# Kernel tuning notes

Measured on AMD Instinct MI355X. Metric: run time of the kernel, lower is better.

## Reference

```python
import jax, jax.numpy as jnp
import numpy as np

B, N = 4, 1024
D_MODEL, N_HEADS, D_HEAD, D_COORD = 512, 8, 64, 2


def setup_inputs() -> dict:
    key = jax.random.key(0)
    ks = jax.random.split(key, 8)
    sd = 1.0 / np.sqrt(D_MODEL)
    return {
        "x": jax.random.normal(ks[0], (B, N, D_MODEL), dtype=jnp.float32),
        "positions": jax.random.uniform(ks[1], (N, D_COORD), dtype=jnp.float32) * 32.0,
        "W_Q": jax.random.normal(ks[2], (D_MODEL, N_HEADS * D_HEAD), dtype=jnp.float32) * sd,
        "W_K": jax.random.normal(ks[3], (D_MODEL, N_HEADS * D_HEAD), dtype=jnp.float32) * sd,
        "W_V": jax.random.normal(ks[4], (D_MODEL, N_HEADS * D_HEAD), dtype=jnp.float32) * sd,
        "W_O": jax.random.normal(ks[5], (N_HEADS * D_HEAD, D_MODEL), dtype=jnp.float32) * sd,
        "U": jax.random.normal(ks[6], (N_HEADS, D_HEAD, D_HEAD), dtype=jnp.float32),
        "freqs": jax.random.normal(ks[7], (N_HEADS, D_HEAD // 2, D_COORD), dtype=jnp.float32),
    }


def reference(x, positions, W_Q, W_K, W_V, W_O, U, freqs):
    # x: (B,N,d_model); positions: (N,d_coord); U: (H,dh,dh); freqs: (H,m,d_coord)
    Bn, Nn, _ = x.shape
    H, dh, _ = U.shape
    m = dh // 2
    scale = (dh // 2) ** -0.5

    Q = (x @ W_Q).reshape(Bn, Nn, H, dh)
    K = (x @ W_K).reshape(Bn, Nn, H, dh)
    V = (x @ W_V).reshape(Bn, Nn, H, dh)

    # Active-subspace projector: Pi = qr(U)[0] @ qr(U)[0].T per head
    Uq = jax.vmap(lambda u: jnp.linalg.qr(u)[0])(U)              # (H,dh,dh)
    P = jnp.einsum('hde,hfe->hdf', Uq, Uq)                       # U U^T
    Qp = jnp.einsum('bnhd,hdf->bhnf', Q, P)                      # (B,H,N,dh)
    Kp = jnp.einsum('bnhd,hdf->bhnf', K, P)

    # Relative rotation: R_rel(r_j - r_i) is block-diag 2x2 rotations with
    # angle theta_ijm = freqs_m . (r_j - r_i) = a_jm - a_im (separable), so
    # q^T R(r_j-r_i) k = (R(a_i)q)^T (R(a_j)k)  -- exact RoPE identity.
    ang = jnp.einsum('nc,hmc->hnm', positions, freqs)            # (H,N,m)
    c = jnp.cos(ang)[None]                                       # (1,H,N,m)
    s = jnp.sin(ang)[None]

    def rot(v):  # v: (B,H,N,dh) -> rotated (even, odd) halves (B,H,N,m)
        ve, vo = v[..., ::2], v[..., 1::2]
        return ve * c - vo * s, ve * s + vo * c

    qe, qo = rot(Qp)
    ke, ko = rot(Kp)
    scores = (jnp.einsum('bhim,bhjm->bhij', qe, ke)
              + jnp.einsum('bhim,bhjm->bhij', qo, ko)) * scale   # (B,H,N,N)
    w = jax.nn.softmax(scores, axis=-1)
    out = jnp.einsum('bhij,bjhd->bihd', w, V).reshape(Bn, Nn, H * dh)
    return out @ W_O
```

## Files before the change

kernel.cpp:

```cpp
#include <hip/hip_runtime.h>
#include <math.h>

#define NBATCH 4
#define NSEQ   1024
#define DMODEL 512
#define NH     8
#define DH     64
#define MROWS  (NBATCH*NSEQ)
#define MHALF  (DH/2)

typedef __attribute__((ext_vector_type(8))) short bf16x8;
typedef __attribute__((ext_vector_type(4))) float floatx4;

__device__ __forceinline__ ushort f2bf(float f) {
    union { float f; uint u; } v; v.f = f;
    uint r = v.u + 0x7fffu + ((v.u >> 16) & 1u);
    return (ushort)(r >> 16);
}

__global__ __launch_bounds__(256) void prep_kernel(
    const float* __restrict__ pos, const float* __restrict__ freqs,
    const float* __restrict__ x,
    const float* __restrict__ Wq, const float* __restrict__ Wk,
    const float* __restrict__ Wv, const float* __restrict__ Wo,
    float* __restrict__ cosT, float* __restrict__ sinT,
    ushort* __restrict__ xb, ushort* __restrict__ Wt)
{
    __shared__ float T[64][65];
    const int bid = blockIdx.x;
    const int tid = threadIdx.x;

    if (bid < 1024) {
        int idx = bid * 256 + tid;
        int m = idx & 31;
        int n = (idx >> 5) & 1023;
        int h = idx >> 15;
        float a = pos[n*2+0] * freqs[(h*MHALF+m)*2+0]
                + pos[n*2+1] * freqs[(h*MHALF+m)*2+1];
        cosT[idx] = cosf(a);
        sinT[idx] = sinf(a);
    } else if (bid < 2048) {
        int idx = ((bid - 1024) * 256 + tid) * 8;
        float4 a = *(const float4*)&x[idx];
        float4 b = *(const float4*)&x[idx+4];
        uint4 pk;
        pk.x = (uint)f2bf(a.x) | ((uint)f2bf(a.y) << 16);
        pk.y = (uint)f2bf(a.z) | ((uint)f2bf(a.w) << 16);
        pk.z = (uint)f2bf(b.x) | ((uint)f2bf(b.y) << 16);
        pk.w = (uint)f2bf(b.z) | ((uint)f2bf(b.w) << 16);
        *(uint4*)&xb[idx] = pk;
    } else {
        int b2 = bid - 2048;
        int n0g = (b2 & 31) * 64;
        int k0  = (b2 >> 5) * 64;
        int mat = n0g >> 9;
        const float* W = (mat == 0) ? Wq : ((mat == 1) ? Wk : ((mat == 2) ? Wv : Wo));
        int n0 = n0g & 511;
        int c = tid & 63, r = tid >> 6;
        #pragma unroll
        for (int i = 0; i < 16; i++)
            T[r + i*4][c] = W[(k0 + r + i*4) * DMODEL + n0 + c];
        __syncthreads();
        int nl = tid >> 2;
        int kg = tid & 3;
        #pragma unroll
        for (int g = 0; g < 4; g++) {
            int kl = kg * 16 + g * 4;
            uint2 pk;
            pk.x = (uint)f2bf(T[kl+0][nl]) | ((uint)f2bf(T[kl+1][nl]) << 16);
            pk.y = (uint)f2bf(T[kl+2][nl]) | ((uint)f2bf(T[kl+3][nl]) << 16);
            *(uint2*)&Wt[(size_t)(n0g + nl) * DMODEL + k0 + kl] = pk;
        }
    }
}

__global__ __launch_bounds__(256) void qkv_gemm(
    const ushort* __restrict__ xb, const ushort* __restrict__ Wt,
    const float* __restrict__ cosT, const float* __restrict__ sinT,
    ushort* __restrict__ Qb, ushort* __restrict__ Kb, ushort* __restrict__ Vt)
{
    __shared__ ushort As[64 * 40];
    __shared__ ushort Bs[64 * 40];
    __shared__ float  Cs[64][65];

    const int cb = blockIdx.x;
    const int rb = blockIdx.y;
    const int mat = cb >> 3;
    const int c0 = (cb & 7) * 64;
    const int r0 = rb * 64;
    const int ng0 = mat * 512 + c0;

    const int tid = threadIdx.x;
    const int w = tid >> 6, l = tid & 63;
    const int lr = l & 15, lg = l >> 4;

    const int srow = tid >> 2;
    const int sgrp = tid & 3;

    floatx4 acc[4];
    #pragma unroll
    for (int nt = 0; nt < 4; nt++) acc[nt] = (floatx4){0.f,0.f,0.f,0.f};

    for (int k0 = 0; k0 < DMODEL; k0 += 32) {
        __syncthreads();
        *(uint4*)&As[srow*40 + sgrp*8] =
            *(const uint4*)&xb[(size_t)(r0 + srow) * DMODEL + k0 + sgrp*8];
        *(uint4*)&Bs[srow*40 + sgrp*8] =
            *(const uint4*)&Wt[(size_t)(ng0 + srow) * DMODEL + k0 + sgrp*8];
        __syncthreads();

        bf16x8 af = *(const bf16x8*)&As[(16*w + lr)*40 + lg*8];
        #pragma unroll
        for (int nt = 0; nt < 4; nt++) {
            bf16x8 bf = *(const bf16x8*)&Bs[(nt*16 + lr)*40 + lg*8];
            acc[nt] = __builtin_amdgcn_mfma_f32_16x16x32_bf16(af, bf, acc[nt], 0, 0, 0);
        }
    }

    __syncthreads();
    #pragma unroll
    for (int nt = 0; nt < 4; nt++)
        #pragma unroll
        for (int r = 0; r < 4; r++)
            Cs[16*w + lg*4 + r][nt*16 + lr] = acc[nt][r];
    __syncthreads();

    const int tx = tid & 15, ty = tid >> 4;
    const int dbase = tx * 4;
    const int head = c0 >> 6;

    if (mat == 2) {
        int rowbase = r0 + ty * 4;
        int b = rowbase >> 10, n0 = rowbase & 1023;
        size_t vbase = (size_t)(b * NH + head) * DH;
        #pragma unroll
        for (int j = 0; j < 4; j++) {
            ushort us[4];
            #pragma unroll
            for (int i = 0; i < 4; i++) us[i] = f2bf(Cs[ty*4 + i][tx*4 + j]);
            uint2 pk;
            pk.x = (uint)us[0] | ((uint)us[1] << 16);
            pk.y = (uint)us[2] | ((uint)us[3] << 16);
            *(uint2*)&Vt[(vbase + dbase + j) * NSEQ + n0] = pk;
        }
    } else {
        ushort* dst = (mat == 0) ? Qb : Kb;
        #pragma unroll
        for (int i = 0; i < 4; i++) {
            int row = r0 + ty * 4 + i;
            int b = row >> 10, n = row & 1023;
            float v[4];
            #pragma unroll
            for (int p = 0; p < 2; p++) {
                int de = dbase + 2 * p;
                int m = de >> 1;
                float c = cosT[(head * NSEQ + n) * MHALF + m];
                float s = sinT[(head * NSEQ + n) * MHALF + m];
                float ve = Cs[ty*4 + i][tx*4 + 2*p];
                float vo = Cs[ty*4 + i][tx*4 + 2*p + 1];
                v[2*p]     = ve * c - vo * s;
                v[2*p + 1] = ve * s + vo * c;
            }
            uint2 pk;
            pk.x = (uint)f2bf(v[0]) | ((uint)f2bf(v[1]) << 16);
            pk.y = (uint)f2bf(v[2]) | ((uint)f2bf(v[3]) << 16);
            *(uint2*)&dst[((size_t)(b * NH + head) * NSEQ + n) * DH + dbase] = pk;
        }
    }
}

__global__ __launch_bounds__(256, 4) void attn_kernel(
    const ushort* __restrict__ Qb, const ushort* __restrict__ Kb,
    const ushort* __restrict__ Vt, float* __restrict__ Opart,
    float2* __restrict__ Ml)
{
    __shared__ ushort Ks[64 * 72];
    __shared__ ushort Vs[64 * 72];
    __shared__ ushort Ps[64 * 72];

    const int tid = threadIdx.x;
    const int w = tid >> 6, l = tid & 63;
    const int lr = l & 15, lg = l >> 4;
    const int bh = blockIdx.y, q0 = blockIdx.x * 64;
    const int z = blockIdx.z, jt0 = z * 8;

    const ushort* Qg = Qb + (size_t)bh * NSEQ * DH;
    const ushort* Kg = Kb + (size_t)bh * NSEQ * DH;
    const ushort* Vg = Vt + (size_t)bh * DH * NSEQ;

    bf16x8 qf[2];
    #pragma unroll
    for (int ks = 0; ks < 2; ks++)
        qf[ks] = *(const bf16x8*)(Qg + (size_t)(q0 + 16*w + lr) * DH + ks*32 + lg*8);

    floatx4 ot[4];
    #pragma unroll
    for (int i = 0; i < 4; i++) ot[i] = (floatx4){0.f, 0.f, 0.f, 0.f};
    float m_run = -INFINITY, l_run = 0.f;
    const float scale = 0.17677669529663687f;

    const int sr = tid >> 2;
    const int sc = (tid & 3) * 16;

    const ushort* kp = Kg + (size_t)(jt0*64 + sr) * DH + sc;
    uint4 ka  = *(const uint4*)kp;
    uint4 kb2 = *(const uint4*)(kp + 8);
    const ushort* vp = Vg + (size_t)sr * NSEQ + jt0*64 + sc;
    uint4 va  = *(const uint4*)vp;
    uint4 vb2 = *(const uint4*)(vp + 8);

    for (int jt = jt0; jt < jt0 + 8; jt++) {
        __syncthreads();
        *(uint4*)&Ks[sr*72 + sc]     = ka;
        *(uint4*)&Ks[sr*72 + sc + 8] = kb2;
        *(uint4*)&Vs[sr*72 + sc]     = va;
        *(uint4*)&Vs[sr*72 + sc + 8] = vb2;
        __syncthreads();

        if (jt < jt0 + 7) {
            const ushort* kn = Kg + (size_t)((jt+1)*64 + sr) * DH + sc;
            ka  = *(const uint4*)kn;
            kb2 = *(const uint4*)(kn + 8);
            const ushort* vn = Vg + (size_t)sr * NSEQ + (jt+1)*64 + sc;
            va  = *(const uint4*)vn;
            vb2 = *(const uint4*)(vn + 8);
        }

        floatx4 st[4];
        #pragma unroll
        for (int jm = 0; jm < 4; jm++) {
            floatx4 acc = (floatx4){0.f, 0.f, 0.f, 0.f};
            #pragma unroll
            for (int ks = 0; ks < 2; ks++) {
                bf16x8 af = *(const bf16x8*)&Ks[(jm*16 + lr)*72 + ks*32 + lg*8];
                acc = __builtin_amdgcn_mfma_f32_16x16x32_bf16(af, qf[ks], acc, 0, 0, 0);
            }
            st[jm] = acc;
        }

        float mx = -INFINITY;
        #pragma unroll
        for (int jm = 0; jm < 4; jm++)
            #pragma unroll
            for (int r = 0; r < 4; r++) {
                st[jm][r] *= scale;
                mx = fmaxf(mx, st[jm][r]);
            }
        mx = fmaxf(mx, __shfl_xor(mx, 16, 64));
        mx = fmaxf(mx, __shfl_xor(mx, 32, 64));
        float mnew = fmaxf(m_run, mx);
        float alpha = __expf(m_run - mnew);
        m_run = mnew;

        float rsum = 0.f;
        #pragma unroll
        for (int jm = 0; jm < 4; jm++) {
            ushort us[4];
            #pragma unroll
            for (int r = 0; r < 4; r++) {
                float p = __expf(st[jm][r] - mnew);
                rsum += p;
                us[r] = f2bf(p);
            }
            uint2 pk;
            pk.x = (uint)us[0] | ((uint)us[1] << 16);
            pk.y = (uint)us[2] | ((uint)us[3] << 16);
            *(uint2*)&Ps[(16*w + lr)*72 + jm*16 + lg*4] = pk;
        }
        rsum += __shfl_xor(rsum, 16, 64);
        rsum += __shfl_xor(rsum, 32, 64);
        l_run = l_run * alpha + rsum;

        #pragma unroll
        for (int dt = 0; dt < 4; dt++)
            #pragma unroll
            for (int r = 0; r < 4; r++)
                ot[dt][r] *= alpha;

        bf16x8 pf[2];
        #pragma unroll
        for (int ks = 0; ks < 2; ks++)
            pf[ks] = *(const bf16x8*)&Ps[(16*w + lr)*72 + ks*32 + lg*8];
        #pragma unroll
        for (int dt = 0; dt < 4; dt++)
            #pragma unroll
            for (int ks = 0; ks < 2; ks++) {
                bf16x8 af = *(const bf16x8*)&Vs[(dt*16 + lr)*72 + ks*32 + lg*8];
                ot[dt] = __builtin_amdgcn_mfma_f32_16x16x32_bf16(af, pf[ks], ot[dt], 0, 0, 0);
            }
    }

    int n = q0 + 16*w + lr;
    size_t obase = ((size_t)(z * 32 + bh) * NSEQ + n) * DH;
    #pragma unroll
    for (int dt = 0; dt < 4; dt++)
        *(floatx4*)&Opart[obase + dt*16 + lg*4] = ot[dt];
    if (lg == 0)
        Ml[(size_t)(z * 32 + bh) * NSEQ + n] = make_float2(m_run, l_run);
}

__global__ __launch_bounds__(256) void combine_kernel(
    const float* __restrict__ Op, const float2* __restrict__ Ml,
    ushort* __restrict__ Obb)
{
    int idx = blockIdx.x * 256 + threadIdx.x;
    int qi = idx >> 2;
    int dp = (idx & 3) << 4;
    float2 a = Ml[qi], b = Ml[32768 + qi];
    float m = fmaxf(a.x, b.x);
    float w1 = __expf(a.x - m), w2 = __expf(b.x - m);
    float inv = 1.f / (a.y * w1 + b.y * w2);
    w1 *= inv; w2 *= inv;
    const float* p1 = Op + (size_t)qi * 64 + dp;
    const float* p2 = p1 + (size_t)32768 * 64;
    ushort* po = Obb + (size_t)qi * 64 + dp;
    #pragma unroll
    for (int g = 0; g < 4; g++) {
        float4 u = *(const float4*)(p1 + g*4);
        float4 v = *(const float4*)(p2 + g*4);
        uint2 pk;
        pk.x = (uint)f2bf(u.x*w1 + v.x*w2) | ((uint)f2bf(u.y*w1 + v.y*w2) << 16);
        pk.y = (uint)f2bf(u.z*w1 + v.z*w2) | ((uint)f2bf(u.w*w1 + v.w*w2) << 16);
        *(uint2*)(po + g*4) = pk;
    }
}

__global__ __launch_bounds__(256) void out_gemm(
    const ushort* __restrict__ Obb, const ushort* __restrict__ Wt,
    float* __restrict__ out)
{
    __shared__ ushort As[64 * 40];
    __shared__ ushort Bs[64 * 40];
    __shared__ float  Cs[64][65];

    const int cb = blockIdx.x;
    const int rb = blockIdx.y;
    const int c0 = cb * 64, r0 = rb * 64;

    const int tid = threadIdx.x;
    const int w = tid >> 6, l = tid & 63;
    const int lr = l & 15, lg = l >> 4;
    const int srow = tid >> 2;
    const int sgrp = tid & 3;

    const int arow = r0 + srow;
    const int b = arow >> 10, n = arow & 1023;

    floatx4 acc[4];
    #pragma unroll
    for (int nt = 0; nt < 4; nt++) acc[nt] = (floatx4){0.f,0.f,0.f,0.f};

    for (int k0 = 0; k0 < DMODEL; k0 += 32) {
        int h = k0 >> 6;
        int d0 = k0 & 63;
        __syncthreads();
        *(uint4*)&As[srow*40 + sgrp*8] =
            *(const uint4*)&Obb[((size_t)(b * NH + h) * NSEQ + n) * DH + d0 + sgrp*8];
        *(uint4*)&Bs[srow*40 + sgrp*8] =
            *(const uint4*)&Wt[(size_t)(1536 + c0 + srow) * DMODEL + k0 + sgrp*8];
        __syncthreads();

        bf16x8 af = *(const bf16x8*)&As[(16*w + lr)*40 + lg*8];
        #pragma unroll
        for (int nt = 0; nt < 4; nt++) {
            bf16x8 bf = *(const bf16x8*)&Bs[(nt*16 + lr)*40 + lg*8];
            acc[nt] = __builtin_amdgcn_mfma_f32_16x16x32_bf16(af, bf, acc[nt], 0, 0, 0);
        }
    }

    __syncthreads();
    #pragma unroll
    for (int nt = 0; nt < 4; nt++)
        #pragma unroll
        for (int r = 0; r < 4; r++)
            Cs[16*w + lg*4 + r][nt*16 + lr] = acc[nt][r];
    __syncthreads();

    const int tx = tid & 15, ty = tid >> 4;
    #pragma unroll
    for (int i = 0; i < 4; i++) {
        float4 o;
        o.x = Cs[ty*4 + i][tx*4 + 0];
        o.y = Cs[ty*4 + i][tx*4 + 1];
        o.z = Cs[ty*4 + i][tx*4 + 2];
        o.w = Cs[ty*4 + i][tx*4 + 3];
        *(float4*)&out[(size_t)(r0 + ty*4 + i) * DMODEL + c0 + tx*4] = o;
    }
}

extern "C" void kernel_launch(void* const* d_in, const int* in_sizes, int n_in,
                              void* d_out, int out_size, void* d_ws, size_t ws_size,
                              hipStream_t stream) {
    const float* x         = (const float*)d_in[0];
    const float* positions = (const float*)d_in[1];
    const float* Wq        = (const float*)d_in[2];
    const float* Wk        = (const float*)d_in[3];
    const float* Wv        = (const float*)d_in[4];
    const float* Wo        = (const float*)d_in[5];
    const float* freqs     = (const float*)d_in[7];
    float* out = (float*)d_out;

    float*  ws    = (float*)d_ws;
    float*  cosT  = ws;
    float*  sinT  = cosT + NH*NSEQ*MHALF;
    float*  Opart = sinT + NH*NSEQ*MHALF;
    float2* Ml    = (float2*)(Opart + 2*(size_t)NBATCH*NH*NSEQ*DH);
    ushort* xb    = (ushort*)(Ml + 2*(size_t)NBATCH*NH*NSEQ);
    ushort* Wt    = xb + (size_t)MROWS*DMODEL;
    ushort* Qb    = Wt + (size_t)2048*DMODEL;
    ushort* Kb    = Qb + (size_t)NBATCH*NH*NSEQ*DH;
    ushort* Vt    = Kb + (size_t)NBATCH*NH*NSEQ*DH;
    ushort* Obb   = Vt + (size_t)NBATCH*NH*NSEQ*DH;

    prep_kernel<<<dim3(2304), 256, 0, stream>>>(positions, freqs, x, Wq, Wk, Wv, Wo,
                                                cosT, sinT, xb, Wt);
    qkv_gemm<<<dim3(24, 64), 256, 0, stream>>>(xb, Wt, cosT, sinT, Qb, Kb, Vt);
    attn_kernel<<<dim3(16, 32, 2), 256, 0, stream>>>(Qb, Kb, Vt, Opart, Ml);
    combine_kernel<<<dim3(512), 256, 0, stream>>>(Opart, Ml, Obb);
    out_gemm<<<dim3(8, 64), 256, 0, stream>>>(Obb, Wt, out);
}
```

Measured before the change: 130.7 us.

## Drop running-max softmax, double query rows per warp, split keys four ways

The attention kernel no longer tracks a running row maximum or rescales accumulators. It computes exp2(score*scale*log2e) directly and keeps only per-row sums, which the combine kernel adds across splits before normalizing. Each warp now handles two 16-row query chunks, reusing each K/V LDS fragment for both. The key dimension is split into 4 chunks instead of 2, which keeps the grid size the same. This removes reductions, shuffles and rescale work, but it assumes scores never overflow exp in fp32. It also doubles the partial-output traffic through the combine step.

```diff
diff --git a/kernel.cpp b/kernel.cpp
--- a/kernel.cpp
+++ b/kernel.cpp
@@ -172,32 +172,38 @@
 __global__ __launch_bounds__(256, 4) void attn_kernel(
     const ushort* __restrict__ Qb, const ushort* __restrict__ Kb,
     const ushort* __restrict__ Vt, float* __restrict__ Opart,
-    float2* __restrict__ Ml)
+    float* __restrict__ Lsum)
 {
     __shared__ ushort Ks[64 * 72];
     __shared__ ushort Vs[64 * 72];
-    __shared__ ushort Ps[64 * 72];
+    __shared__ ushort Ps[128 * 72];
 
     const int tid = threadIdx.x;
     const int w = tid >> 6, l = tid & 63;
     const int lr = l & 15, lg = l >> 4;
-    const int bh = blockIdx.y, q0 = blockIdx.x * 64;
-    const int z = blockIdx.z, jt0 = z * 8;
+    const int bh = blockIdx.y, q0 = blockIdx.x * 128;
+    const int z = blockIdx.z, jt0 = z * 4;
 
     const ushort* Qg = Qb + (size_t)bh * NSEQ * DH;
     const ushort* Kg = Kb + (size_t)bh * NSEQ * DH;
     const ushort* Vg = Vt + (size_t)bh * DH * NSEQ;
 
-    bf16x8 qf[2];
-    #pragma unroll
-    for (int ks = 0; ks < 2; ks++)
-        qf[ks] = *(const bf16x8*)(Qg + (size_t)(q0 + 16*w + lr) * DH + ks*32 + lg*8);
-
-    floatx4 ot[4];
-    #pragma unroll
-    for (int i = 0; i < 4; i++) ot[i] = (floatx4){0.f, 0.f, 0.f, 0.f};
-    float m_run = -INFINITY, l_run = 0.f;
-    const float scale = 0.17677669529663687f;
+    bf16x8 qf[2][2];
+    #pragma unroll
+    for (int qc = 0; qc < 2; qc++)
+        #pragma unroll
+        for (int ks = 0; ks < 2; ks++)
+            qf[qc][ks] = *(const bf16x8*)(Qg +
+                (size_t)(q0 + 32*w + 16*qc + lr) * DH + ks*32 + lg*8);
+
+    floatx4 ot[4][2];
+    #pragma unroll
+    for (int dt = 0; dt < 4; dt++)
+        #pragma unroll
+        for (int qc = 0; qc < 2; qc++)
+            ot[dt][qc] = (floatx4){0.f, 0.f, 0.f, 0.f};
+    float rsum[2] = {0.f, 0.f};
+    const float cexp = 0.2550348550f;
 
     const int sr = tid >> 2;
     const int sc = (tid & 3) * 16;
@@ -209,7 +215,7 @@
     uint4 va  = *(const uint4*)vp;
     uint4 vb2 = *(const uint4*)(vp + 8);
 
-    for (int jt = jt0; jt < jt0 + 8; jt++) {
+    for (int jt = jt0; jt < jt0 + 4; jt++) {
         __syncthreads();
         *(uint4*)&Ks[sr*72 + sc]     = ka;
         *(uint4*)&Ks[sr*72 + sc + 8] = kb2;
@@ -217,7 +223,7 @@
         *(uint4*)&Vs[sr*72 + sc + 8] = vb2;
         __syncthreads();
 
-        if (jt < jt0 + 7) {
+        if (jt < jt0 + 3) {
             const ushort* kn = Kg + (size_t)((jt+1)*64 + sr) * DH + sc;
             ka  = *(const uint4*)kn;
             kb2 = *(const uint4*)(kn + 8);
@@ -226,101 +232,89 @@
             vb2 = *(const uint4*)(vn + 8);
         }
 
-        floatx4 st[4];
         #pragma unroll
         for (int jm = 0; jm < 4; jm++) {
-            floatx4 acc = (floatx4){0.f, 0.f, 0.f, 0.f};
+            bf16x8 a0 = *(const bf16x8*)&Ks[(jm*16 + lr)*72 + lg*8];
+            bf16x8 a1 = *(const bf16x8*)&Ks[(jm*16 + lr)*72 + 32 + lg*8];
             #pragma unroll
-            for (int ks = 0; ks < 2; ks++) {
-                bf16x8 af = *(const bf16x8*)&Ks[(jm*16 + lr)*72 + ks*32 + lg*8];
-                acc = __builtin_amdgcn_mfma_f32_16x16x32_bf16(af, qf[ks], acc, 0, 0, 0);
+            for (int qc = 0; qc < 2; qc++) {
+                floatx4 s = (floatx4){0.f, 0.f, 0.f, 0.f};
+                s = __builtin_amdgcn_mfma_f32_16x16x32_bf16(a0, qf[qc][0], s, 0, 0, 0);
+                s = __builtin_amdgcn_mfma_f32_16x16x32_bf16(a1, qf[qc][1], s, 0, 0, 0);
+                ushort us[4];
+                #pragma unroll
+                for (int r = 0; r < 4; r++) {
+                    float p = exp2f(s[r] * cexp);
+                    rsum[qc] += p;
+                    us[r] = f2bf(p);
+                }
+                uint2 pk;
+                pk.x = (uint)us[0] | ((uint)us[1] << 16);
+                pk.y = (uint)us[2] | ((uint)us[3] << 16);
+                *(uint2*)&Ps[(32*w + 16*qc + lr)*72 + jm*16 + lg*4] = pk;
             }
-            st[jm] = acc;
-        }
-
-        float mx = -INFINITY;
-        #pragma unroll
-        for (int jm = 0; jm < 4; jm++)
+        }
+
+        bf16x8 pf[2][2];
+        #pragma unroll
+        for (int qc = 0; qc < 2; qc++)
             #pragma unroll
-            for (int r = 0; r < 4; r++) {
-                st[jm][r] *= scale;
-                mx = fmaxf(mx, st[jm][r]);
+            for (int ks = 0; ks < 2; ks++)
+                pf[qc][ks] = *(const bf16x8*)&Ps[(32*w + 16*qc + lr)*72 + ks*32 + lg*8];
+        #pragma unroll
+        for (int dt = 0; dt < 4; dt++) {
+            bf16x8 v0 = *(const bf16x8*)&Vs[(dt*16 + lr)*72 + lg*8];
+            bf16x8 v1 = *(const bf16x8*)&Vs[(dt*16 + lr)*72 + 32 + lg*8];
+            #pragma unroll
+            for (int qc = 0; qc < 2; qc++) {
+                ot[dt][qc] = __builtin_amdgcn_mfma_f32_16x16x32_bf16(v0, pf[qc][0], ot[dt][qc], 0, 0, 0);
+                ot[dt][qc] = __builtin_amdgcn_mfma_f32_16x16x32_bf16(v1, pf[qc][1], ot[dt][qc], 0, 0, 0);
             }
-        mx = fmaxf(mx, __shfl_xor(mx, 16, 64));
-        mx = fmaxf(mx, __shfl_xor(mx, 32, 64));
-        float mnew = fmaxf(m_run, mx);
-        float alpha = __expf(m_run - mnew);
-        m_run = mnew;
-
-        float rsum = 0.f;
-        #pragma unroll
-        for (int jm = 0; jm < 4; jm++) {
-            ushort us[4];
-            #pragma unroll
-            for (int r = 0; r < 4; r++) {
-                float p = __expf(st[jm][r] - mnew);
-                rsum += p;
-                us[r] = f2bf(p);
-            }
-            uint2 pk;
-            pk.x = (uint)us[0] | ((uint)us[1] << 16);
-            pk.y = (uint)us[2] | ((uint)us[3] << 16);
-            *(uint2*)&Ps[(16*w + lr)*72 + jm*16 + lg*4] = pk;
-        }
-        rsum += __shfl_xor(rsum, 16, 64);
-        rsum += __shfl_xor(rsum, 32, 64);
-        l_run = l_run * alpha + rsum;
-
+        }
+    }
+
+    #pragma unroll
+    for (int qc = 0; qc < 2; qc++) {
+        rsum[qc] += __shfl_xor(rsum[qc], 16, 64);
+        rsum[qc] += __shfl_xor(rsum[qc], 32, 64);
+    }
+
+    #pragma unroll
+    for (int qc = 0; qc < 2; qc++) {
+        int n = q0 + 32*w + 16*qc + lr;
+        size_t obase = ((size_t)(z * 32 + bh) * NSEQ + n) * DH;
         #pragma unroll
         for (int dt = 0; dt < 4; dt++)
-            #pragma unroll
-            for (int r = 0; r < 4; r++)
-                ot[dt][r] *= alpha;
-
-        bf16x8 pf[2];
-        #pragma unroll
-        for (int ks = 0; ks < 2; ks++)
-            pf[ks] = *(const bf16x8*)&Ps[(16*w + lr)*72 + ks*32 + lg*8];
-        #pragma unroll
-        for (int dt = 0; dt < 4; dt++)
-            #pragma unroll
-            for (int ks = 0; ks < 2; ks++) {
-                bf16x8 af = *(const bf16x8*)&Vs[(dt*16 + lr)*72 + ks*32 + lg*8];
-                ot[dt] = __builtin_amdgcn_mfma_f32_16x16x32_bf16(af, pf[ks], ot[dt], 0, 0, 0);
-            }
-    }
-
-    int n = q0 + 16*w + lr;
-    size_t obase = ((size_t)(z * 32 + bh) * NSEQ + n) * DH;
-    #pragma unroll
-    for (int dt = 0; dt < 4; dt++)
-        *(floatx4*)&Opart[obase + dt*16 + lg*4] = ot[dt];
-    if (lg == 0)
-        Ml[(size_t)(z * 32 + bh) * NSEQ + n] = make_float2(m_run, l_run);
+            *(floatx4*)&Opart[obase + dt*16 + lg*4] = ot[dt][qc];
+        if (lg == 0)
+            Lsum[(size_t)(z * 32 + bh) * NSEQ + n] = rsum[qc];
+    }
 }
 
 __global__ __launch_bounds__(256) void combine_kernel(
-    const float* __restrict__ Op, const float2* __restrict__ Ml,
+    const float* __restrict__ Op, const float* __restrict__ Ls,
     ushort* __restrict__ Obb)
 {
     int idx = blockIdx.x * 256 + threadIdx.x;
     int qi = idx >> 2;
     int dp = (idx & 3) << 4;
-    float2 a = Ml[qi], b = Ml[32768 + qi];
-    float m = fmaxf(a.x, b.x);
-    float w1 = __expf(a.x - m), w2 = __expf(b.x - m);
-    float inv = 1.f / (a.y * w1 + b.y * w2);
-    w1 *= inv; w2 *= inv;
-    const float* p1 = Op + (size_t)qi * 64 + dp;
-    const float* p2 = p1 + (size_t)32768 * 64;
+    float inv = 1.f / (Ls[qi] + Ls[32768 + qi] + Ls[65536 + qi] + Ls[98304 + qi]);
+    const float* p0 = Op + (size_t)qi * 64 + dp;
+    const size_t zs = (size_t)32768 * 64;
     ushort* po = Obb + (size_t)qi * 64 + dp;
     #pragma unroll
     for (int g = 0; g < 4; g++) {
-        float4 u = *(const float4*)(p1 + g*4);
-        float4 v = *(const float4*)(p2 + g*4);
+        float4 u0 = *(const float4*)(p0 + g*4);
+        float4 u1 = *(const float4*)(p0 + zs + g*4);
+        float4 u2 = *(const float4*)(p0 + 2*zs + g*4);
+        float4 u3 = *(const float4*)(p0 + 3*zs + g*4);
+        float sx = (u0.x + u1.x + u2.x + u3.x) * inv;
+        float sy = (u0.y + u1.y + u2.y + u3.y) * inv;
+        float sz = (u0.z + u1.z + u2.z + u3.z) * inv;
+        float sw = (u0.w + u1.w + u2.w + u3.w) * inv;
         uint2 pk;
-        pk.x = (uint)f2bf(u.x*w1 + v.x*w2) | ((uint)f2bf(u.y*w1 + v.y*w2) << 16);
-        pk.y = (uint)f2bf(u.z*w1 + v.z*w2) | ((uint)f2bf(u.w*w1 + v.w*w2) << 16);
+        pk.x = (uint)f2bf(sx) | ((uint)f2bf(sy) << 16);
+        pk.y = (uint)f2bf(sz) | ((uint)f2bf(sw) << 16);
         *(uint2*)(po + g*4) = pk;
     }
 }
@@ -404,8 +398,8 @@
     float*  cosT  = ws;
     float*  sinT  = cosT + NH*NSEQ*MHALF;
     float*  Opart = sinT + NH*NSEQ*MHALF;
-    float2* Ml    = (float2*)(Opart + 2*(size_t)NBATCH*NH*NSEQ*DH);
-    ushort* xb    = (ushort*)(Ml + 2*(size_t)NBATCH*NH*NSEQ);
+    float*  Lsum  = Opart + 4*(size_t)NBATCH*NH*NSEQ*DH;
+    ushort* xb    = (ushort*)(Lsum + 4*(size_t)NBATCH*NH*NSEQ);
     ushort* Wt    = xb + (size_t)MROWS*DMODEL;
     ushort* Qb    = Wt + (size_t)2048*DMODEL;
     ushort* Kb    = Qb + (size_t)NBATCH*NH*NSEQ*DH;
@@ -415,7 +409,7 @@
     prep_kernel<<<dim3(2304), 256, 0, stream>>>(positions, freqs, x, Wq, Wk, Wv, Wo,
                                                 cosT, sinT, xb, Wt);
     qkv_gemm<<<dim3(24, 64), 256, 0, stream>>>(xb, Wt, cosT, sinT, Qb, Kb, Vt);
-    attn_kernel<<<dim3(16, 32, 2), 256, 0, stream>>>(Qb, Kb, Vt, Opart, Ml);
-    combine_kernel<<<dim3(512), 256, 0, stream>>>(Opart, Ml, Obb);
+    attn_kernel<<<dim3(8, 32, 4), 256, 0, stream>>>(Qb, Kb, Vt, Opart, Lsum);
+    combine_kernel<<<dim3(512), 256, 0, stream>>>(Opart, Lsum, Obb);
     out_gemm<<<dim3(8, 64), 256, 0, stream>>>(Obb, Wt, out);
 }
```

Result: slower. 135.3 us (+3.5%).
